# Optimization experiments

Hardware: AMD Instinct MI355X
Metric: run time of the kernel (lower is better)

The kernel has to match this reference:

```python
import jax, jax.numpy as jnp
import numpy as np

TEMPERATURE = 8.0  # sqrt(head_dim=64)
NEG_BIG = -10000.0


def setup_inputs() -> dict:
    key = jax.random.key(0)
    kq, kk, kv, km = jax.random.split(key, 4)
    B, H, S, D, K = 4, 8, 1024, 64, 4
    q = jax.random.normal(kq, (B, H, S, D), dtype=jnp.float32)
    k = jax.random.normal(kk, (B, H, S, D), dtype=jnp.float32)
    v = jax.random.normal(kv, (B, H, S, D), dtype=jnp.float32)
    # K binary attention masks, broadcastable to [B,H,S,S]
    mask = jax.random.randint(km, (K, 1, 1, S, S), 0, 2).astype(jnp.float32)
    return {"q": q, "k": k, "v": v, "mask": mask}


def reference(q, k, v, mask):
    # attn: [B,H,S,S]
    attn = jnp.einsum("bhsd,bhtd->bhst", q / TEMPERATURE, k)
    # additive mask: [K,1,1,S,S]
    ext_mask = (1.0 - mask) * NEG_BIG
    # batched over K instead of the original python loop: [K,B,H,S,S]
    probs = jax.nn.softmax(attn[None] + ext_mask, axis=-1)
    # dropout is identity in eval mode (deterministic reference)
    output = jnp.einsum("kbhst,bhtd->kbhsd", probs, v)
    return (output, attn)
```

## Files before the change

kernel.cpp:

```cpp
#include <hip/hip_runtime.h>
#include <hip/hip_bf16.h>
#include <stdint.h>

typedef float f4 __attribute__((ext_vector_type(4)));
typedef short bf8 __attribute__((ext_vector_type(8)));
typedef uint32_t u4 __attribute__((ext_vector_type(4)));

#define SDIM 1024
#define DDIM 64
#define NBH  32
#define KM   4
#define NT   16

__device__ __forceinline__ unsigned short f2bf(float f) {
  uint32_t u = __builtin_bit_cast(uint32_t, f);
  u += 0x7fffu + ((u >> 16) & 1u);
  return (unsigned short)(u >> 16);
}

#define GLOAD16(gsrc, ldst)                                                  \
  __builtin_amdgcn_global_load_lds(                                          \
      (const __attribute__((address_space(1))) unsigned int*)(gsrc),         \
      (__attribute__((address_space(3))) unsigned int*)(ldst), 16, 0, 0)

__device__ __forceinline__ bf8 lds_ld(const unsigned short* base, int row, int e0) {
  return *(const bf8*)((const char*)base + (((row * 64 + e0) * 2) ^ ((row & 7) << 4)));
}

__global__ __launch_bounds__(256) void conv_qk(const float* __restrict__ q,
                                               const float* __restrict__ k,
                                               unsigned short* __restrict__ qb,
                                               unsigned short* __restrict__ kb, int n8) {
  int i = blockIdx.x * 256 + threadIdx.x;
  const float* src = q;
  unsigned short* dst = qb;
  float scale = 0.125f;
  int j = i;
  if (i >= n8) { src = k; dst = kb; scale = 1.0f; j = i - n8; }
  int base = j * 8;
  f4 a = *(const f4*)(src + base);
  f4 b = *(const f4*)(src + base + 4);
  bf8 o;
  o[0] = (short)f2bf(a[0] * scale); o[1] = (short)f2bf(a[1] * scale);
  o[2] = (short)f2bf(a[2] * scale); o[3] = (short)f2bf(a[3] * scale);
  o[4] = (short)f2bf(b[0] * scale); o[5] = (short)f2bf(b[1] * scale);
  o[6] = (short)f2bf(b[2] * scale); o[7] = (short)f2bf(b[3] * scale);
  *(bf8*)(dst + base) = o;
}

__global__ __launch_bounds__(256) void transp_v(const float* __restrict__ v,
                                                unsigned short* __restrict__ vt) {
  __shared__ float tv[64][65];
  int bh = blockIdx.x >> 4;
  int s0 = (blockIdx.x & 15) * 64;
  int t = threadIdx.x;
  int sr = t >> 2, c0 = (t & 3) * 16;
  const float* vp = v + ((size_t)(bh * SDIM) + s0 + sr) * DDIM + c0;
#pragma unroll
  for (int i = 0; i < 4; ++i) {
    f4 x = *(const f4*)(vp + 4 * i);
#pragma unroll
    for (int j = 0; j < 4; ++j) tv[sr][c0 + 4 * i + j] = x[j];
  }
  __syncthreads();
  int d = t >> 2, sc0 = (t & 3) * 16;
  unsigned short tmp[16];
#pragma unroll
  for (int i = 0; i < 16; ++i) tmp[i] = f2bf(tv[sc0 + i][d]);
  unsigned short* op = vt + ((size_t)(bh * DDIM) + d) * SDIM + s0 + sc0;
  bf8 o0, o1;
#pragma unroll
  for (int j = 0; j < 8; ++j) { o0[j] = (short)tmp[j]; o1[j] = (short)tmp[j + 8]; }
  *(bf8*)(op) = o0;
  *(bf8*)(op + 8) = o1;
}

__global__ __launch_bounds__(256) void mask_to_bits(const float* __restrict__ mask,
                                                    uint32_t* __restrict__ mb2) {
  int gid = blockIdx.x * 256 + threadIdx.x;
  float mv = mask[gid];
  unsigned long long bal = __ballot(mv > 0.5f);
  int lane = threadIdx.x & 63;
  int m = gid >> 20;
  int r = (gid >> 10) & 1023;
  int c = gid & 1023;
  if (lane == 0)       mb2[m * 32768 + (c >> 5) * 1024 + r] = (uint32_t)bal;
  else if (lane == 32) mb2[m * 32768 + (c >> 5) * 1024 + r] = (uint32_t)(bal >> 32);
}

__global__ __launch_bounds__(512, 4) void attn_main(
    const unsigned short* __restrict__ qb, const unsigned short* __restrict__ kb,
    const unsigned short* __restrict__ vtg, const uint32_t* __restrict__ mb2,
    float* __restrict__ outO, float* __restrict__ attn) {
  __shared__ __align__(16) unsigned short q_s[64 * 64];
  __shared__ __align__(16) unsigned short k_s[2][64 * 64];
  __shared__ __align__(16) unsigned short v_s[2][64 * 64];
  __shared__ __align__(16) unsigned short e_s[64 * 64];

  const int tid = threadIdx.x;
  const int l   = tid & 63;
  const int w   = tid >> 6;
  const int m   = w >> 1;
  const int h   = w & 1;
  const int l16 = l & 15;
  const int lg  = l >> 4;

  int bid = (int)blockIdx.x;
  bid = (bid & 7) * 64 + (bid >> 3);
  const int bh = bid >> 4;
  const int r0 = (bid & 15) * 64;

  const int srow = tid >> 3;
  const int sd   = ((tid & 7) ^ (srow & 7)) << 3;
  const unsigned short* qsrc = qb  + ((size_t)(bh * SDIM) + r0 + srow) * DDIM + sd;
  const unsigned short* ksrc = kb  + ((size_t)(bh * SDIM) + srow) * DDIM + sd;
  const unsigned short* vsrc = vtg + ((size_t)(bh * DDIM) + srow) * SDIM + sd;

  GLOAD16(qsrc, &q_s[tid * 8]);
  GLOAD16(ksrc, &k_s[0][tid * 8]);
  GLOAD16(vsrc, &v_s[0][tid * 8]);

  f4 acc[2][4] = {};
  f4 accl[2]   = {};
  bf8 ones;
#pragma unroll
  for (int b = 0; b < 8; ++b) ones[b] = (short)0x3F80;

  const uint32_t* mbase = mb2 + m * 32768 + r0 + l16;

  for (int ct = 0; ct < NT; ++ct) {
    const int cur = ct & 1;
    __syncthreads();

    uint32_t mdw[2][2];
#pragma unroll
    for (int mt2 = 0; mt2 < 2; ++mt2)
#pragma unroll
      for (int kt = 0; kt < 2; ++kt)
        mdw[mt2][kt] = mbase[(ct * 2 + kt) * 1024 + 16 * (2 * h + mt2)];

    {
      const int qr  = 16 * m + l16;
      const int kc0 = 32 * h + l16;
      bf8 a0  = lds_ld(q_s, qr, lg * 8);
      bf8 a1  = lds_ld(q_s, qr, lg * 8 + 32);
      bf8 b00 = lds_ld(k_s[cur], kc0,      lg * 8);
      bf8 b01 = lds_ld(k_s[cur], kc0,      lg * 8 + 32);
      bf8 b10 = lds_ld(k_s[cur], kc0 + 16, lg * 8);
      bf8 b11 = lds_ld(k_s[cur], kc0 + 16, lg * 8 + 32);
      f4 s0 = {}, s1 = {};
      s0 = __builtin_amdgcn_mfma_f32_16x16x32_bf16(a0, b00, s0, 0, 0, 0);
      s0 = __builtin_amdgcn_mfma_f32_16x16x32_bf16(a1, b01, s0, 0, 0, 0);
      s1 = __builtin_amdgcn_mfma_f32_16x16x32_bf16(a0, b10, s1, 0, 0, 0);
      s1 = __builtin_amdgcn_mfma_f32_16x16x32_bf16(a1, b11, s1, 0, 0, 0);

      float* arow = attn + ((size_t)(bh * SDIM) + r0 + 16 * m + 4 * lg) * SDIM
                    + ct * 64 + 32 * h + l16;
#pragma unroll
      for (int j = 0; j < 2; ++j) {
        f4 sv = j ? s1 : s0;
#pragma unroll
        for (int r = 0; r < 4; ++r) {
          arow[(size_t)r * SDIM + 16 * j] = sv[r];
          int row = 16 * m + 4 * lg + r;
          int col = 32 * h + 16 * j + l16;
          *(unsigned short*)((char*)e_s + (((row * 64 + col) * 2) ^ ((row & 7) << 4)))
              = f2bf(__expf(sv[r]));
        }
      }
    }
    __syncthreads();

    if (ct + 1 < NT) {
      const int nxt = cur ^ 1;
      GLOAD16(ksrc + (size_t)(ct + 1) * 4096, &k_s[nxt][tid * 8]);
      GLOAD16(vsrc + (size_t)(ct + 1) * 64,   &v_s[nxt][tid * 8]);
    }

    {
      bf8 af[2][2];
#pragma unroll
      for (int mt2 = 0; mt2 < 2; ++mt2) {
        const int row = 16 * (2 * h + mt2) + l16;
#pragma unroll
        for (int kt = 0; kt < 2; ++kt) {
          bf8 e = lds_ld(e_s, row, kt * 32 + lg * 8);
          uint32_t bits = (mdw[mt2][kt] >> (lg * 8)) & 0xffu;
          u4 ew = __builtin_bit_cast(u4, e);
#pragma unroll
          for (int d = 0; d < 4; ++d) {
            uint32_t n2 = (bits >> (2 * d)) & 3u;
            uint32_t sp = (n2 * 0x8001u) & 0x00010001u;
            ew[d] &= (sp << 16) - sp;
          }
          af[mt2][kt] = __builtin_bit_cast(bf8, ew);
        }
        accl[mt2] = __builtin_amdgcn_mfma_f32_16x16x32_bf16(af[mt2][0], ones, accl[mt2], 0, 0, 0);
        accl[mt2] = __builtin_amdgcn_mfma_f32_16x16x32_bf16(af[mt2][1], ones, accl[mt2], 0, 0, 0);
      }
#pragma unroll
      for (int nt = 0; nt < 4; ++nt) {
        const int dc = 16 * nt + l16;
        bf8 bv0 = lds_ld(v_s[cur], dc, lg * 8);
        bf8 bv1 = lds_ld(v_s[cur], dc, lg * 8 + 32);
#pragma unroll
        for (int mt2 = 0; mt2 < 2; ++mt2) {
          acc[mt2][nt] = __builtin_amdgcn_mfma_f32_16x16x32_bf16(af[mt2][0], bv0, acc[mt2][nt], 0, 0, 0);
          acc[mt2][nt] = __builtin_amdgcn_mfma_f32_16x16x32_bf16(af[mt2][1], bv1, acc[mt2][nt], 0, 0, 0);
        }
      }
    }
  }

#pragma unroll
  for (int mt2 = 0; mt2 < 2; ++mt2) {
#pragma unroll
    for (int r = 0; r < 4; ++r) {
      float inv = 1.0f / accl[mt2][r];
      int row = 16 * (2 * h + mt2) + 4 * lg + r;
      float* orow = outO + (((size_t)(m * NBH + bh)) * SDIM + r0 + row) * DDIM + l16;
#pragma unroll
      for (int nt = 0; nt < 4; ++nt)
        orow[16 * nt] = acc[mt2][nt][r] * inv;
    }
  }
}

extern "C" void kernel_launch(void* const* d_in, const int* in_sizes, int n_in,
                              void* d_out, int out_size, void* d_ws, size_t ws_size,
                              hipStream_t stream) {
  (void)in_sizes; (void)n_in; (void)out_size; (void)ws_size;
  const float* q    = (const float*)d_in[0];
  const float* k    = (const float*)d_in[1];
  const float* v    = (const float*)d_in[2];
  const float* mask = (const float*)d_in[3];
  float* outO = (float*)d_out;
  float* attn = (float*)d_out + (size_t)KM * NBH * SDIM * DDIM;

  char* ws = (char*)d_ws;
  unsigned short* qb = (unsigned short*)ws;
  unsigned short* kb = (unsigned short*)(ws + (4u << 20));
  unsigned short* vt = (unsigned short*)(ws + (8u << 20));
  uint32_t*       mb = (uint32_t*)(ws + (12u << 20));

  const int n  = NBH * SDIM * DDIM;
  const int n8 = n / 8;
  conv_qk<<<2 * n8 / 256, 256, 0, stream>>>(q, k, qb, kb, n8);
  transp_v<<<NBH * 16, 256, 0, stream>>>(v, vt);
  mask_to_bits<<<(KM * SDIM * SDIM) / 256, 256, 0, stream>>>(mask, mb);
  attn_main<<<NBH * 16, 512, 0, stream>>>(qb, kb, vt, mb, outO, attn);
}
```

Measured before the change: 61.65 us.

## Merge prepass kernels, fuse Q conversion, and split attention into 32-row blocks

```diff
diff --git a/kernel.cpp b/kernel.cpp
--- a/kernel.cpp
+++ b/kernel.cpp
@@ -5,6 +5,7 @@
 typedef float f4 __attribute__((ext_vector_type(4)));
 typedef short bf8 __attribute__((ext_vector_type(8)));
 typedef uint32_t u4 __attribute__((ext_vector_type(4)));
+typedef uint32_t u2 __attribute__((ext_vector_type(2)));
 
 #define SDIM 1024
 #define DDIM 64
@@ -12,6 +13,10 @@
 #define KM   4
 #define NT   16
 
+#define MB_BLK 16384
+#define KB_BLK 1024
+#define VT_BLK 512
+
 __device__ __forceinline__ unsigned short f2bf(float f) {
   uint32_t u = __builtin_bit_cast(uint32_t, f);
   u += 0x7fffu + ((u >> 16) & 1u);
@@ -27,98 +32,105 @@
   return *(const bf8*)((const char*)base + (((row * 64 + e0) * 2) ^ ((row & 7) << 4)));
 }
 
-__global__ __launch_bounds__(256) void conv_qk(const float* __restrict__ q,
-                                               const float* __restrict__ k,
-                                               unsigned short* __restrict__ qb,
-                                               unsigned short* __restrict__ kb, int n8) {
-  int i = blockIdx.x * 256 + threadIdx.x;
-  const float* src = q;
-  unsigned short* dst = qb;
-  float scale = 0.125f;
-  int j = i;
-  if (i >= n8) { src = k; dst = kb; scale = 1.0f; j = i - n8; }
-  int base = j * 8;
-  f4 a = *(const f4*)(src + base);
-  f4 b = *(const f4*)(src + base + 4);
-  bf8 o;
-  o[0] = (short)f2bf(a[0] * scale); o[1] = (short)f2bf(a[1] * scale);
-  o[2] = (short)f2bf(a[2] * scale); o[3] = (short)f2bf(a[3] * scale);
-  o[4] = (short)f2bf(b[0] * scale); o[5] = (short)f2bf(b[1] * scale);
-  o[6] = (short)f2bf(b[2] * scale); o[7] = (short)f2bf(b[3] * scale);
-  *(bf8*)(dst + base) = o;
-}
-
-__global__ __launch_bounds__(256) void transp_v(const float* __restrict__ v,
-                                                unsigned short* __restrict__ vt) {
+__global__ __launch_bounds__(256) void prepass(
+    const float* __restrict__ k, const float* __restrict__ v,
+    const float* __restrict__ mask, unsigned short* __restrict__ kb,
+    unsigned short* __restrict__ vt, uint32_t* __restrict__ mb2) {
   __shared__ float tv[64][65];
-  int bh = blockIdx.x >> 4;
-  int s0 = (blockIdx.x & 15) * 64;
-  int t = threadIdx.x;
-  int sr = t >> 2, c0 = (t & 3) * 16;
-  const float* vp = v + ((size_t)(bh * SDIM) + s0 + sr) * DDIM + c0;
-#pragma unroll
-  for (int i = 0; i < 4; ++i) {
-    f4 x = *(const f4*)(vp + 4 * i);
-#pragma unroll
-    for (int j = 0; j < 4; ++j) tv[sr][c0 + 4 * i + j] = x[j];
-  }
-  __syncthreads();
-  int d = t >> 2, sc0 = (t & 3) * 16;
-  unsigned short tmp[16];
-#pragma unroll
-  for (int i = 0; i < 16; ++i) tmp[i] = f2bf(tv[sc0 + i][d]);
-  unsigned short* op = vt + ((size_t)(bh * DDIM) + d) * SDIM + s0 + sc0;
-  bf8 o0, o1;
-#pragma unroll
-  for (int j = 0; j < 8; ++j) { o0[j] = (short)tmp[j]; o1[j] = (short)tmp[j + 8]; }
-  *(bf8*)(op) = o0;
-  *(bf8*)(op + 8) = o1;
-}
-
-__global__ __launch_bounds__(256) void mask_to_bits(const float* __restrict__ mask,
-                                                    uint32_t* __restrict__ mb2) {
-  int gid = blockIdx.x * 256 + threadIdx.x;
-  float mv = mask[gid];
-  unsigned long long bal = __ballot(mv > 0.5f);
-  int lane = threadIdx.x & 63;
-  int m = gid >> 20;
-  int r = (gid >> 10) & 1023;
-  int c = gid & 1023;
-  if (lane == 0)       mb2[m * 32768 + (c >> 5) * 1024 + r] = (uint32_t)bal;
-  else if (lane == 32) mb2[m * 32768 + (c >> 5) * 1024 + r] = (uint32_t)(bal >> 32);
-}
-
-__global__ __launch_bounds__(512, 4) void attn_main(
-    const unsigned short* __restrict__ qb, const unsigned short* __restrict__ kb,
+  const int b = blockIdx.x;
+  const int t = threadIdx.x;
+  if (b < MB_BLK) {
+    int gid = b * 256 + t;
+    float mv = mask[gid];
+    unsigned long long bal = __ballot(mv > 0.5f);
+    int lane = t & 63;
+    int m = gid >> 20;
+    int r = (gid >> 10) & 1023;
+    int c = gid & 1023;
+    if (lane == 0)       mb2[m * 32768 + (c >> 5) * 1024 + r] = (uint32_t)bal;
+    else if (lane == 32) mb2[m * 32768 + (c >> 5) * 1024 + r] = (uint32_t)(bal >> 32);
+  } else if (b < MB_BLK + KB_BLK) {
+    int base = ((b - MB_BLK) * 256 + t) * 8;
+    f4 a = *(const f4*)(k + base);
+    f4 c = *(const f4*)(k + base + 4);
+    bf8 o;
+    o[0] = (short)f2bf(a[0]); o[1] = (short)f2bf(a[1]);
+    o[2] = (short)f2bf(a[2]); o[3] = (short)f2bf(a[3]);
+    o[4] = (short)f2bf(c[0]); o[5] = (short)f2bf(c[1]);
+    o[6] = (short)f2bf(c[2]); o[7] = (short)f2bf(c[3]);
+    *(bf8*)(kb + base) = o;
+  } else {
+    int vb = b - MB_BLK - KB_BLK;
+    int bh = vb >> 4;
+    int s0 = (vb & 15) * 64;
+    int sr = t >> 2, c0 = (t & 3) * 16;
+    const float* vp = v + ((size_t)(bh * SDIM) + s0 + sr) * DDIM + c0;
+#pragma unroll
+    for (int i = 0; i < 4; ++i) {
+      f4 x = *(const f4*)(vp + 4 * i);
+#pragma unroll
+      for (int j = 0; j < 4; ++j) tv[sr][c0 + 4 * i + j] = x[j];
+    }
+    __syncthreads();
+    int d = t >> 2, sc0 = (t & 3) * 16;
+    unsigned short tmp[16];
+#pragma unroll
+    for (int i = 0; i < 16; ++i) tmp[i] = f2bf(tv[sc0 + i][d]);
+    unsigned short* op = vt + ((size_t)(bh * DDIM) + d) * SDIM + s0 + sc0;
+    bf8 o0, o1;
+#pragma unroll
+    for (int j = 0; j < 8; ++j) { o0[j] = (short)tmp[j]; o1[j] = (short)tmp[j + 8]; }
+    *(bf8*)(op) = o0;
+    *(bf8*)(op + 8) = o1;
+  }
+}
+
+__global__ __launch_bounds__(256, 4) void attn_main(
+    const float* __restrict__ qf, const unsigned short* __restrict__ kb,
     const unsigned short* __restrict__ vtg, const uint32_t* __restrict__ mb2,
     float* __restrict__ outO, float* __restrict__ attn) {
-  __shared__ __align__(16) unsigned short q_s[64 * 64];
+  __shared__ __align__(16) unsigned short q_s[32 * 64];
   __shared__ __align__(16) unsigned short k_s[2][64 * 64];
   __shared__ __align__(16) unsigned short v_s[2][64 * 64];
-  __shared__ __align__(16) unsigned short e_s[64 * 64];
+  __shared__ __align__(16) unsigned short e_s[32 * 64];
 
   const int tid = threadIdx.x;
   const int l   = tid & 63;
   const int w   = tid >> 6;
-  const int m   = w >> 1;
-  const int h   = w & 1;
   const int l16 = l & 15;
   const int lg  = l >> 4;
+  const int wh  = w & 1;
+  const int wc  = w >> 1;
 
   int bid = (int)blockIdx.x;
-  bid = (bid & 7) * 64 + (bid >> 3);
-  const int bh = bid >> 4;
-  const int r0 = (bid & 15) * 64;
+  bid = (bid & 7) * 128 + (bid >> 3);
+  const int bh = bid >> 5;
+  const int r0 = (bid & 31) * 32;
 
   const int srow = tid >> 3;
   const int sd   = ((tid & 7) ^ (srow & 7)) << 3;
-  const unsigned short* qsrc = qb  + ((size_t)(bh * SDIM) + r0 + srow) * DDIM + sd;
-  const unsigned short* ksrc = kb  + ((size_t)(bh * SDIM) + srow) * DDIM + sd;
-  const unsigned short* vsrc = vtg + ((size_t)(bh * DDIM) + srow) * SDIM + sd;
-
-  GLOAD16(qsrc, &q_s[tid * 8]);
-  GLOAD16(ksrc, &k_s[0][tid * 8]);
-  GLOAD16(vsrc, &v_s[0][tid * 8]);
+  const unsigned short* ksrc0 = kb  + ((size_t)(bh * SDIM) + srow) * DDIM + sd;
+  const unsigned short* ksrc1 = kb  + ((size_t)(bh * SDIM) + srow + 32) * DDIM + sd;
+  const unsigned short* vsrc0 = vtg + ((size_t)(bh * DDIM) + srow) * SDIM + sd;
+  const unsigned short* vsrc1 = vtg + ((size_t)(bh * DDIM) + srow + 32) * SDIM + sd;
+
+  GLOAD16(ksrc0, &k_s[0][tid * 8]);
+  GLOAD16(ksrc1, &k_s[0][(tid + 256) * 8]);
+  GLOAD16(vsrc0, &v_s[0][tid * 8]);
+  GLOAD16(vsrc1, &v_s[0][(tid + 256) * 8]);
+
+  {
+    int row = tid >> 3, d0 = (tid & 7) * 8;
+    const float* qp = qf + ((size_t)(bh * SDIM) + r0 + row) * DDIM + d0;
+    f4 a = *(const f4*)qp;
+    f4 c = *(const f4*)(qp + 4);
+    bf8 o;
+    o[0] = (short)f2bf(a[0] * 0.125f); o[1] = (short)f2bf(a[1] * 0.125f);
+    o[2] = (short)f2bf(a[2] * 0.125f); o[3] = (short)f2bf(a[3] * 0.125f);
+    o[4] = (short)f2bf(c[0] * 0.125f); o[5] = (short)f2bf(c[1] * 0.125f);
+    o[6] = (short)f2bf(c[2] * 0.125f); o[7] = (short)f2bf(c[3] * 0.125f);
+    *(bf8*)((char*)q_s + (((row * 64 + d0) * 2) ^ ((row & 7) << 4))) = o;
+  }
 
   f4 acc[2][4] = {};
   f4 accl[2]   = {};
@@ -126,62 +138,64 @@
 #pragma unroll
   for (int b = 0; b < 8; ++b) ones[b] = (short)0x3F80;
 
-  const uint32_t* mbase = mb2 + m * 32768 + r0 + l16;
+  const uint32_t* mbase = mb2 + w * 32768 + r0 + l16;
+
+  __syncthreads();
 
   for (int ct = 0; ct < NT; ++ct) {
     const int cur = ct & 1;
-    __syncthreads();
 
     uint32_t mdw[2][2];
 #pragma unroll
     for (int mt2 = 0; mt2 < 2; ++mt2)
 #pragma unroll
       for (int kt = 0; kt < 2; ++kt)
-        mdw[mt2][kt] = mbase[(ct * 2 + kt) * 1024 + 16 * (2 * h + mt2)];
+        mdw[mt2][kt] = mbase[(ct * 2 + kt) * 1024 + 16 * mt2];
 
     {
-      const int qr  = 16 * m + l16;
-      const int kc0 = 32 * h + l16;
-      bf8 a0  = lds_ld(q_s, qr, lg * 8);
-      bf8 a1  = lds_ld(q_s, qr, lg * 8 + 32);
-      bf8 b00 = lds_ld(k_s[cur], kc0,      lg * 8);
-      bf8 b01 = lds_ld(k_s[cur], kc0,      lg * 8 + 32);
-      bf8 b10 = lds_ld(k_s[cur], kc0 + 16, lg * 8);
-      bf8 b11 = lds_ld(k_s[cur], kc0 + 16, lg * 8 + 32);
-      f4 s0 = {}, s1 = {};
-      s0 = __builtin_amdgcn_mfma_f32_16x16x32_bf16(a0, b00, s0, 0, 0, 0);
-      s0 = __builtin_amdgcn_mfma_f32_16x16x32_bf16(a1, b01, s0, 0, 0, 0);
-      s1 = __builtin_amdgcn_mfma_f32_16x16x32_bf16(a0, b10, s1, 0, 0, 0);
-      s1 = __builtin_amdgcn_mfma_f32_16x16x32_bf16(a1, b11, s1, 0, 0, 0);
-
-      float* arow = attn + ((size_t)(bh * SDIM) + r0 + 16 * m + 4 * lg) * SDIM
-                    + ct * 64 + 32 * h + l16;
+      const int qr = 16 * wh + l16;
+      bf8 bq0 = lds_ld(q_s, qr, lg * 8);
+      bf8 bq1 = lds_ld(q_s, qr, lg * 8 + 32);
+      f4 s[2];
 #pragma unroll
       for (int j = 0; j < 2; ++j) {
-        f4 sv = j ? s1 : s0;
-#pragma unroll
-        for (int r = 0; r < 4; ++r) {
-          arow[(size_t)r * SDIM + 16 * j] = sv[r];
-          int row = 16 * m + 4 * lg + r;
-          int col = 32 * h + 16 * j + l16;
-          *(unsigned short*)((char*)e_s + (((row * 64 + col) * 2) ^ ((row & 7) << 4)))
-              = f2bf(__expf(sv[r]));
-        }
+        const int kc = 32 * wc + 16 * j + l16;
+        bf8 ak0 = lds_ld(k_s[cur], kc, lg * 8);
+        bf8 ak1 = lds_ld(k_s[cur], kc, lg * 8 + 32);
+        f4 sv = {};
+        sv = __builtin_amdgcn_mfma_f32_16x16x32_bf16(ak0, bq0, sv, 0, 0, 0);
+        sv = __builtin_amdgcn_mfma_f32_16x16x32_bf16(ak1, bq1, sv, 0, 0, 0);
+        s[j] = sv;
+      }
+      float* arow = attn + ((size_t)(bh * SDIM) + r0 + 16 * wh + l16) * SDIM
+                    + ct * 64 + 32 * wc + 4 * lg;
+      *(f4*)(arow)      = s[0];
+      *(f4*)(arow + 16) = s[1];
+      const int erow = 16 * wh + l16;
+#pragma unroll
+      for (int j = 0; j < 2; ++j) {
+        u2 ev;
+        ev[0] = (uint32_t)f2bf(__expf(s[j][0])) | ((uint32_t)f2bf(__expf(s[j][1])) << 16);
+        ev[1] = (uint32_t)f2bf(__expf(s[j][2])) | ((uint32_t)f2bf(__expf(s[j][3])) << 16);
+        int col = 32 * wc + 16 * j + 4 * lg;
+        *(u2*)((char*)e_s + (((erow * 64 + col) * 2) ^ ((erow & 7) << 4))) = ev;
       }
     }
     __syncthreads();
 
     if (ct + 1 < NT) {
       const int nxt = cur ^ 1;
-      GLOAD16(ksrc + (size_t)(ct + 1) * 4096, &k_s[nxt][tid * 8]);
-      GLOAD16(vsrc + (size_t)(ct + 1) * 64,   &v_s[nxt][tid * 8]);
+      GLOAD16(ksrc0 + (size_t)(ct + 1) * 4096, &k_s[nxt][tid * 8]);
+      GLOAD16(ksrc1 + (size_t)(ct + 1) * 4096, &k_s[nxt][(tid + 256) * 8]);
+      GLOAD16(vsrc0 + (size_t)(ct + 1) * 64,   &v_s[nxt][tid * 8]);
+      GLOAD16(vsrc1 + (size_t)(ct + 1) * 64,   &v_s[nxt][(tid + 256) * 8]);
     }
 
     {
       bf8 af[2][2];
 #pragma unroll
       for (int mt2 = 0; mt2 < 2; ++mt2) {
-        const int row = 16 * (2 * h + mt2) + l16;
+        const int row = 16 * mt2 + l16;
 #pragma unroll
         for (int kt = 0; kt < 2; ++kt) {
           bf8 e = lds_ld(e_s, row, kt * 32 + lg * 8);
@@ -210,6 +224,7 @@
         }
       }
     }
+    __syncthreads();
   }
 
 #pragma unroll
@@ -217,8 +232,8 @@
 #pragma unroll
     for (int r = 0; r < 4; ++r) {
       float inv = 1.0f / accl[mt2][r];
-      int row = 16 * (2 * h + mt2) + 4 * lg + r;
-      float* orow = outO + (((size_t)(m * NBH + bh)) * SDIM + r0 + row) * DDIM + l16;
+      int row = 16 * mt2 + 4 * lg + r;
+      float* orow = outO + (((size_t)(w * NBH + bh)) * SDIM + r0 + row) * DDIM + l16;
 #pragma unroll
       for (int nt = 0; nt < 4; ++nt)
         orow[16 * nt] = acc[mt2][nt][r] * inv;
@@ -238,15 +253,10 @@
   float* attn = (float*)d_out + (size_t)KM * NBH * SDIM * DDIM;
 
   char* ws = (char*)d_ws;
-  unsigned short* qb = (unsigned short*)ws;
-  unsigned short* kb = (unsigned short*)(ws + (4u << 20));
-  unsigned short* vt = (unsigned short*)(ws + (8u << 20));
-  uint32_t*       mb = (uint32_t*)(ws + (12u << 20));
-
-  const int n  = NBH * SDIM * DDIM;
-  const int n8 = n / 8;
-  conv_qk<<<2 * n8 / 256, 256, 0, stream>>>(q, k, qb, kb, n8);
-  transp_v<<<NBH * 16, 256, 0, stream>>>(v, vt);
-  mask_to_bits<<<(KM * SDIM * SDIM) / 256, 256, 0, stream>>>(mask, mb);
-  attn_main<<<NBH * 16, 512, 0, stream>>>(qb, kb, vt, mb, outO, attn);
-}
+  unsigned short* kb = (unsigned short*)ws;
+  unsigned short* vt = (unsigned short*)(ws + (4u << 20));
+  uint32_t*       mb = (uint32_t*)(ws + (8u << 20));
+
+  prepass<<<MB_BLK + KB_BLK + VT_BLK, 256, 0, stream>>>(k, v, mask, kb, vt, mb);
+  attn_main<<<NBH * 32, 256, 0, stream>>>(q, kb, vt, mb, outO, attn);
+}
```

Result: faster. 57.56 us (-6.6%).
